# Performance work log

Hardware: AMD Instinct MI355X
Metric: run time of the kernel (lower is better)

The kernel has to match this reference:

```python
import jax, jax.numpy as jnp
import numpy as np

B, S, D, H = 4, 1024, 1024, 16
HS = D // H  # head_size = 64


def setup_inputs() -> dict:
    key = jax.random.key(0)
    ks = jax.random.split(key, 6)
    scale = 1.0 / np.sqrt(D)
    data = jax.random.normal(ks[0], (B, S, D), dtype=jnp.float32)
    # Per-head projection weights, stacked: [H, D, HS] (no bias, per nn.Linear(bias=False))
    Wq = jax.random.normal(ks[1], (H, D, HS), dtype=jnp.float32) * scale
    Wk = jax.random.normal(ks[2], (H, D, HS), dtype=jnp.float32) * scale
    Wv = jax.random.normal(ks[3], (H, D, HS), dtype=jnp.float32) * scale
    # Output projection: [H*HS, D] plus bias [D]
    Wo = jax.random.normal(ks[4], (H * HS, D), dtype=jnp.float32) * scale
    bo = jax.random.normal(ks[5], (D,), dtype=jnp.float32) * 0.01
    return {"data": data, "Wq": Wq, "Wk": Wk, "Wv": Wv, "Wo": Wo, "bo": bo}


def reference(data, Wq, Wk, Wv, Wo, bo):
    b, s, d = data.shape
    # Per-head Q/K/V projections (self-attention: encoder_data = data)
    q = jnp.einsum('bsd,hde->bhse', data, Wq)  # [B,H,S,HS]
    k = jnp.einsum('bsd,hde->bhse', data, Wk)
    v = jnp.einsum('bsd,hde->bhse', data, Wv)
    # NOTE: original scales by sqrt(embedding_dimension), not sqrt(head_size)
    scores = jnp.einsum('bhse,bhte->bhst', q, k) / jnp.sqrt(jnp.asarray(d, dtype=data.dtype))
    # causal mask (tril of block_size, sliced to [S, S])
    causal = jnp.tril(jnp.ones((s, s), dtype=bool))
    scores = jnp.where(causal, scores, -jnp.inf)
    attn = jax.nn.softmax(scores, axis=-1)  # dropout rate 0.0 -> identity
    out = jnp.einsum('bhst,bhte->bhse', attn, v)  # [B,H,S,HS]
    # concat heads along feature dim (head order matches ModuleList order)
    out = out.transpose(0, 2, 1, 3).reshape(b, s, -1)  # [B,S,H*HS]
    return out @ Wo + bo
```

## Files before the change

kernel.cpp:

```cpp
#include <hip/hip_runtime.h>
#include <hip/hip_bf16.h>
#include <stdint.h>

#define NEG_SENTINEL (-1e30f)

typedef short s16x8 __attribute__((ext_vector_type(8)));
typedef float f32x4 __attribute__((ext_vector_type(4)));
typedef float f32x16 __attribute__((ext_vector_type(16)));

__device__ __forceinline__ ushort f2bf(float f) {
  union { float f; uint32_t u; } v; v.f = f;
  uint32_t u = v.u;
  u += 0x7fffu + ((u >> 16) & 1u);
  return (ushort)(u >> 16);
}
__device__ __forceinline__ ushort f2bf_rn(float f) {
  union { float f; uint32_t u; } v; v.f = f;
  return (ushort)((v.u + 0x8000u) >> 16);
}

__device__ __forceinline__ uint32_t pk_bf16(float lo, float hi) {
  uint32_t r;
  asm("v_cvt_pk_bf16_f32 %0, %1, %2" : "=v"(r) : "v"(lo), "v"(hi));
  return r;
}

__device__ __forceinline__ void async_ld16(ushort* lds, const ushort* g) {
  __builtin_amdgcn_global_load_lds(
      (const __attribute__((address_space(1))) uint32_t*)g,
      (__attribute__((address_space(3))) uint32_t*)lds, 16, 0, 0);
}

__global__ __launch_bounds__(256) void convert_f32_bf16(
    const float* __restrict__ src, ushort* __restrict__ dst) {
  long i = ((long)blockIdx.x * 256 + threadIdx.x) * 8;
  float4 a = *(const float4*)(src + i);
  float4 b = *(const float4*)(src + i + 4);
  union { ushort u[8]; uint4 v; } o;
  o.u[0] = f2bf(a.x); o.u[1] = f2bf(a.y); o.u[2] = f2bf(a.z); o.u[3] = f2bf(a.w);
  o.u[4] = f2bf(b.x); o.u[5] = f2bf(b.y); o.u[6] = f2bf(b.z); o.u[7] = f2bf(b.w);
  *(uint4*)(dst + i) = o.v;
}

__global__ __launch_bounds__(256) void transpose_w3(
    const float* __restrict__ Wq, const float* __restrict__ Wk,
    const float* __restrict__ Wv, ushort* __restrict__ WTall) {
  const int z = blockIdx.z;
  const int matsel = z >> 4;
  const float* src = (matsel == 0 ? Wq : (matsel == 1 ? Wk : Wv)) +
                     (long)(z & 15) * 65536;
  ushort* dst = WTall + (long)z * 65536;
  const int it = blockIdx.y;
  __shared__ __align__(16) ushort tile[64 * 72];
  const int tid = threadIdx.x;
#pragma unroll
  for (int p = 0; p < 4; ++p) {
    int chunk = tid + p * 256;
    int r = chunk >> 4, c0 = (chunk & 15) * 4;
    float4 f = *(const float4*)(src + (long)(it * 64 + r) * 64 + c0);
    union { ushort u[4]; uint2 v; } o;
    o.u[0] = f2bf(f.x); o.u[1] = f2bf(f.y); o.u[2] = f2bf(f.z); o.u[3] = f2bf(f.w);
    *(uint2*)&tile[r * 72 + c0] = o.v;
  }
  __syncthreads();
#pragma unroll
  for (int p = 0; p < 2; ++p) {
    int chunk = tid + p * 256;
    int r = chunk >> 3, c0 = (chunk & 7) * 8;
    union { ushort u[8]; uint4 v; } tmp;
#pragma unroll
    for (int k2 = 0; k2 < 8; ++k2) tmp.u[k2] = tile[(c0 + k2) * 72 + r];
    *(uint4*)(dst + (long)r * 1024 + it * 64 + c0) = tmp.v;
  }
}

__global__ __launch_bounds__(256) void transpose_cvt(
    const float* __restrict__ src, ushort* __restrict__ dst) {
  const int jt = blockIdx.x;
  const int it = blockIdx.y;
  __shared__ __align__(16) ushort tile[64 * 72];
  const int tid = threadIdx.x;
#pragma unroll
  for (int p = 0; p < 4; ++p) {
    int chunk = tid + p * 256;
    int r = chunk >> 4, c0 = (chunk & 15) * 4;
    float4 f = *(const float4*)(src + (long)(it * 64 + r) * 1024 + jt * 64 + c0);
    union { ushort u[4]; uint2 v; } o;
    o.u[0] = f2bf(f.x); o.u[1] = f2bf(f.y); o.u[2] = f2bf(f.z); o.u[3] = f2bf(f.w);
    *(uint2*)&tile[r * 72 + c0] = o.v;
  }
  __syncthreads();
#pragma unroll
  for (int p = 0; p < 2; ++p) {
    int chunk = tid + p * 256;
    int r = chunk >> 3, c0 = (chunk & 7) * 8;
    union { ushort u[8]; uint4 v; } tmp;
#pragma unroll
    for (int k2 = 0; k2 < 8; ++k2) tmp.u[k2] = tile[(c0 + k2) * 72 + r];
    *(uint4*)(dst + (long)(jt * 64 + r) * 1024 + it * 64 + c0) = tmp.v;
  }
}

__device__ __forceinline__ void gemm_core_128x128(
    const ushort* __restrict__ A, const ushort* __restrict__ BT,
    ushort* As, ushort* Bs, f32x4 acc[4][4]) {
  const int tid = threadIdx.x;
  const int lane = tid & 63, w = tid >> 6, quad = lane >> 4, l15 = lane & 15;
  const int wm = w >> 1, wn = w & 1;
  for (int k0 = 0; k0 < 1024; k0 += 64) {
#pragma unroll
    for (int p = 0; p < 4; ++p) {
      int c = tid + p * 256;
      int r = c >> 3, c8 = (c & 7) * 8;
      async_ld16(As + c * 8, A + (long)r * 1024 + k0 + c8);
      async_ld16(Bs + c * 8, BT + (long)r * 1024 + k0 + c8);
    }
    __syncthreads();
#pragma unroll
    for (int kk = 0; kk < 64; kk += 32) {
      s16x8 af[4], bfr[4];
#pragma unroll
      for (int mi = 0; mi < 4; ++mi)
        af[mi] = *(const s16x8*)&As[(wm * 64 + mi * 16 + l15) * 64 + kk + quad * 8];
#pragma unroll
      for (int ni = 0; ni < 4; ++ni)
        bfr[ni] = *(const s16x8*)&Bs[(wn * 64 + ni * 16 + l15) * 64 + kk + quad * 8];
#pragma unroll
      for (int mi = 0; mi < 4; ++mi)
#pragma unroll
        for (int ni = 0; ni < 4; ++ni)
          acc[mi][ni] = __builtin_amdgcn_mfma_f32_16x16x32_bf16(
              af[mi], bfr[ni], acc[mi][ni], 0, 0, 0);
    }
    __syncthreads();
  }
}

#define BAR() do { asm volatile("" ::: "memory"); \
  __builtin_amdgcn_s_barrier(); \
  asm volatile("" ::: "memory"); } while (0)
#define LGKM0() do { asm volatile("s_waitcnt lgkmcnt(0)" ::: "memory"); \
  __builtin_amdgcn_sched_barrier(0); } while (0)
#define STAGE2(LDSB, G) do { \
  async_ld16((LDSB) + o0, (G) + so0); \
  async_ld16((LDSB) + o0 + 4096, (G) + so0 + 65536); } while (0)
#define LD_A(PA, MIB) do { \
  _Pragma("unroll") for (int dm = 0; dm < 4; ++dm) { \
    afr[dm][0] = *(const s16x8*)((PA) + ((MIB) + dm) * 1024); \
    afr[dm][1] = *(const s16x8*)((PA) + ((MIB) + dm) * 1024 + 512); } } while (0)
#define LD_B(PB, NIB) do { \
  _Pragma("unroll") for (int dn = 0; dn < 2; ++dn) { \
    bfr[(NIB) + dn][0] = *(const s16x8*)((PB) + ((NIB) + dn) * 1024); \
    bfr[(NIB) + dn][1] = *(const s16x8*)((PB) + ((NIB) + dn) * 1024 + 512); } } while (0)
#define MFMA_Q(MIB, NIB) do { \
  __builtin_amdgcn_s_setprio(1); \
  _Pragma("unroll") for (int kg = 0; kg < 2; ++kg) \
    _Pragma("unroll") for (int dm = 0; dm < 4; ++dm) \
      _Pragma("unroll") for (int dn = 0; dn < 2; ++dn) \
        acc[(MIB) + dm][(NIB) + dn] = __builtin_amdgcn_mfma_f32_16x16x32_bf16( \
            afr[dm][kg], bfr[(NIB) + dn][kg], acc[(MIB) + dm][(NIB) + dn], 0, 0, 0); \
  __builtin_amdgcn_s_setprio(0); } while (0)

__global__ __launch_bounds__(512, 2) void qkv_proj256(
    const ushort* __restrict__ dataB, const ushort* __restrict__ WTall,
    ushort* __restrict__ QKV) {
  __shared__ __align__(16) ushort smem[65536];
  const int tid = threadIdx.x;
  const int lane = tid & 63, w = tid >> 6, quad = lane >> 4, l15 = lane & 15;
  const int wm = w >> 2, wn = w & 3;
  const int m0 = blockIdx.x * 256;
  const int n0 = blockIdx.y * 256;

  const int o0 = tid * 8;
  const int st_ = o0 >> 9, u_ = o0 & 511;
  const int u0_ = u_ ^ (((u_ >> 8) & 1) << 4);
  const long so0 = (long)((st_ >> 1) * 16 + (u0_ >> 5)) * 1024 +
                   (st_ & 1) * 32 + (u0_ & 31);

  const ushort* Ab = dataB + (long)m0 * 1024;
  const ushort* Bb = WTall + (long)n0 * 1024;

  const int alane = (l15 * 32 + quad * 8) ^ (((l15 >> 3) & 1) << 4);
  const ushort* pA0 = smem + wm * 8192 + alane;
  const ushort* pB0 = smem + 16384 + (wn >> 1) * 8192 + (wn & 1) * 4096 + alane;
  const ushort* pA1 = pA0 + 32768;
  const ushort* pB1 = pB0 + 32768;

  f32x4 acc[8][4];
  const f32x4 z = {0.f, 0.f, 0.f, 0.f};
#pragma unroll
  for (int mi = 0; mi < 8; ++mi)
#pragma unroll
    for (int ni = 0; ni < 4; ++ni) acc[mi][ni] = z;

  s16x8 afr[4][2];
  s16x8 bfr[4][2];

  STAGE2(smem + 16384, Bb);
  STAGE2(smem + 16384 + 8192, Bb + 131072);
  STAGE2(smem, Ab);
  STAGE2(smem + 8192, Ab + 131072);
  STAGE2(smem + 32768 + 16384, Bb + 64);
  STAGE2(smem + 32768 + 16384 + 8192, Bb + 131072 + 64);
  asm volatile("s_waitcnt vmcnt(4)" ::: "memory");
  BAR();

#pragma unroll 1
  for (int it = 0; it < 8; ++it) {
    const int t0k = it * 128;
    const bool sN = (it < 7);
    LD_A(pA0, 0); LD_B(pB0, 0);
    STAGE2(smem + 32768, Ab + t0k + 64);
    asm volatile("s_waitcnt lgkmcnt(8)" ::: "memory");
    BAR(); LGKM0();
    MFMA_Q(0, 0);
    BAR();
    LD_B(pB0, 2);
    STAGE2(smem + 32768 + 8192, Ab + 131072 + t0k + 64);
    BAR(); LGKM0();
    MFMA_Q(0, 2);
    BAR();
    LD_A(pA0, 4);
    if (sN) STAGE2(smem + 16384, Bb + t0k + 128);
    BAR(); LGKM0();
    MFMA_Q(4, 0);
    BAR();
    if (sN) STAGE2(smem + 16384 + 8192, Bb + 131072 + t0k + 128);
    BAR(); LGKM0();
    MFMA_Q(4, 2);
    if (sN) { asm volatile("s_waitcnt vmcnt(4)" ::: "memory"); }
    else    { asm volatile("s_waitcnt vmcnt(0)" ::: "memory"); }
    BAR();
    LD_A(pA1, 0); LD_B(pB1, 0);
    if (sN) STAGE2(smem, Ab + t0k + 128);
    asm volatile("s_waitcnt lgkmcnt(8)" ::: "memory");
    BAR(); LGKM0();
    MFMA_Q(0, 0);
    BAR();
    LD_B(pB1, 2);
    if (sN) STAGE2(smem + 8192, Ab + 131072 + t0k + 128);
    BAR(); LGKM0();
    MFMA_Q(0, 2);
    BAR();
    LD_A(pA1, 4);
    if (sN) STAGE2(smem + 32768 + 16384, Bb + t0k + 192);
    BAR(); LGKM0();
    MFMA_Q(4, 0);
    BAR();
    if (sN) STAGE2(smem + 32768 + 16384 + 8192, Bb + 131072 + t0k + 192);
    BAR(); LGKM0();
    MFMA_Q(4, 2);
    if (sN) {
      asm volatile("s_waitcnt vmcnt(4)" ::: "memory");
      BAR();
    }
  }

  const int matsel = n0 >> 10;
  const int bI = m0 >> 10, s0 = m0 & 1023;
  const int nloc0 = (n0 & 1023) + wn * 64;
  if (matsel < 2) {
    const float sc = (matsel == 0) ? 0.04508422f : 1.0f;
    ushort* base = QKV + (long)matsel * 4194304 + (long)bI * 1048576;
#pragma unroll
    for (int mi = 0; mi < 8; ++mi) {
#pragma unroll
      for (int ni = 0; ni < 4; ++ni) {
        int n = nloc0 + ni * 16 + l15;
        int h = n >> 6, e = n & 63;
        int sb = s0 + wm * 128 + mi * 16 + quad * 4;
        ushort* p = base + (long)h * 65536 + (sb >> 5) * 2048 + (e >> 4) * 512 +
                    ((e >> 3) & 1) * 256 + (sb & 31) * 8 + (e & 7);
#pragma unroll
        for (int i = 0; i < 4; ++i)
          p[i * 8] = f2bf(acc[mi][ni][i] * sc);
      }
    }
  } else {
    ushort* base = QKV + 8388608 + (long)bI * 1048576;
#pragma unroll
    for (int mi = 0; mi < 8; ++mi) {
#pragma unroll
      for (int ni = 0; ni < 4; ++ni) {
        int n = nloc0 + ni * 16 + l15;
        int h = n >> 6, e = n & 63;
        int sb = s0 + wm * 128 + mi * 16 + quad * 4;
        union { ushort u[4]; uint2 v; } o;
#pragma unroll
        for (int i = 0; i < 4; ++i) o.u[i] = f2bf(acc[mi][ni][i]);
        *(uint2*)(base + (long)h * 65536 + (sb >> 5) * 2048 +
                  ((e >> 5) + 2 * ((sb >> 4) & 1)) * 512 +
                  ((e & 31) + 32 * ((sb >> 3) & 1)) * 8 + (sb & 7)) = o.v;
      }
    }
  }
}

__global__ __launch_bounds__(256) void out_proj(
    const ushort* __restrict__ Ocat, const ushort* __restrict__ WoT,
    const float* __restrict__ bo, float* __restrict__ out) {
  __shared__ __align__(16) ushort As[128 * 64];
  __shared__ __align__(16) ushort Bs[128 * 64];
  const int m0 = blockIdx.x * 128;
  const int n0 = blockIdx.y * 128;
  f32x4 acc[4][4];
  const f32x4 z = {0.f, 0.f, 0.f, 0.f};
#pragma unroll
  for (int mi = 0; mi < 4; ++mi)
#pragma unroll
    for (int ni = 0; ni < 4; ++ni) acc[mi][ni] = z;
  gemm_core_128x128(Ocat + (long)m0 * 1024, WoT + (long)n0 * 1024, As, Bs, acc);

  const int tid = threadIdx.x;
  const int lane = tid & 63, w = tid >> 6, quad = lane >> 4, l15 = lane & 15;
  const int wm = w >> 1, wn = w & 1;
#pragma unroll
  for (int mi = 0; mi < 4; ++mi) {
#pragma unroll
    for (int ni = 0; ni < 4; ++ni) {
#pragma unroll
      for (int i = 0; i < 4; ++i) {
        int m = m0 + wm * 64 + mi * 16 + quad * 4 + i;
        int n = n0 + wn * 64 + ni * 16 + l15;
        out[(long)m * 1024 + n] = acc[mi][ni][i] + bo[n];
      }
    }
  }
}

__global__ __launch_bounds__(256, 2) void attn_kernel(
    const ushort* __restrict__ QKV, ushort* __restrict__ Ocat) {
  const int x = blockIdx.x;
  const int tid = threadIdx.x;
  const int w = tid >> 6;
  const int lane = tid & 63, l31 = lane & 31, hi = lane >> 5;
  const int c = (x < 256) ? (31 - (x >> 4)) : ((x - 256) >> 4);
  const int bh = (x & 15) * 4 + w;
  const int b = bh >> 4, h = bh & 15;
  const int q0 = c * 32;

  const ushort* Qp = QKV + (long)bh * 65536;
  const ushort* Kp = QKV + 4194304 + (long)bh * 65536;
  const ushort* VTp = QKV + 8388608 + (long)bh * 65536;

  s16x8 qf[4];
#pragma unroll
  for (int es = 0; es < 4; ++es)
    qf[es] = *(const s16x8*)(Qp + c * 2048 + es * 512 + lane * 8);

  f32x16 oacc0, oacc1;
#pragma unroll
  for (int r = 0; r < 16; ++r) { oacc0[r] = 0.f; oacc1[r] = 0.f; }
  float l_part = 0.f;
  const int nsub = c + 1;

  s16x8 kc[4], vc[4], kn[4], vn[4];
#pragma unroll
  for (int es = 0; es < 4; ++es)
    kc[es] = *(const s16x8*)(Kp + es * 512 + lane * 8);
#pragma unroll
  for (int t = 0; t < 4; ++t)
    vc[t] = *(const s16x8*)(VTp + t * 512 + lane * 8);

  for (int s = 0;; ++s) {
    const bool last = (s + 1 >= nsub);
    if (!last) {
#pragma unroll
      for (int es = 0; es < 4; ++es)
        kn[es] = *(const s16x8*)(Kp + (s + 1) * 2048 + es * 512 + lane * 8);
#pragma unroll
      for (int t = 0; t < 4; ++t)
        vn[t] = *(const s16x8*)(VTp + (s + 1) * 2048 + t * 512 + lane * 8);
    }
    f32x16 sacc;
#pragma unroll
    for (int r = 0; r < 16; ++r) sacc[r] = 0.f;
#pragma unroll
    for (int es = 0; es < 4; ++es)
      sacc = __builtin_amdgcn_mfma_f32_32x32x16_bf16(kc[es], qf[es], sacc,
                                                     0, 0, 0);
    if (s == c) {
#pragma unroll
      for (int r = 0; r < 16; ++r) {
        int kvoff = (r & 3) + 8 * (r >> 2) + 4 * hi;
        if (kvoff > l31) sacc[r] = NEG_SENTINEL;
      }
    }
    float ex[16];
#pragma unroll
    for (int r = 0; r < 16; ++r) { ex[r] = exp2f(sacc[r]); l_part += ex[r]; }
    uint32_t xw[8], yw[8];
#pragma unroll
    for (int k = 0; k < 8; ++k) xw[k] = pk_bf16(ex[2 * k], ex[2 * k + 1]);
#pragma unroll
    for (int k = 0; k < 8; ++k)
      yw[k] = (uint32_t)__shfl_xor((int)xw[k], 32, 64);
#pragma unroll
    for (int win = 0; win < 2; ++win) {
      const int bs = 4 * win;
      union { uint32_t u[4]; s16x8 v; } pa;
      pa.u[0] = hi ? yw[bs + 2] : xw[bs + 0];
      pa.u[1] = hi ? yw[bs + 3] : xw[bs + 1];
      pa.u[2] = hi ? xw[bs + 2] : yw[bs + 0];
      pa.u[3] = hi ? xw[bs + 3] : yw[bs + 1];
      oacc0 = __builtin_amdgcn_mfma_f32_32x32x16_bf16(pa.v, vc[win * 2 + 0],
                                                      oacc0, 0, 0, 0);
      oacc1 = __builtin_amdgcn_mfma_f32_32x32x16_bf16(pa.v, vc[win * 2 + 1],
                                                      oacc1, 0, 0, 0);
    }
    if (last) break;
#pragma unroll
    for (int es = 0; es < 4; ++es) kc[es] = kn[es];
#pragma unroll
    for (int t = 0; t < 4; ++t) vc[t] = vn[t];
  }

  float l_tot = l_part + __shfl_xor(l_part, 32, 64);

  ushort* Ob = Ocat + ((long)(b * 1024 + q0) * 1024) + h * 64;
#pragma unroll
  for (int r = 0; r < 16; ++r) {
    int qloc = (r & 3) + 8 * (r >> 2) + 4 * hi;
    float lv = __shfl(l_tot, qloc, 64);
    float linv = __builtin_amdgcn_rcpf(lv > 1e-30f ? lv : 1.0f);
    Ob[(long)qloc * 1024 + l31] = f2bf_rn(oacc0[r] * linv);
    Ob[(long)qloc * 1024 + 32 + l31] = f2bf_rn(oacc1[r] * linv);
  }
}

extern "C" void kernel_launch(void* const* d_in, const int* in_sizes, int n_in,
                              void* d_out, int out_size, void* d_ws, size_t ws_size,
                              hipStream_t stream) {
  const float* data = (const float*)d_in[0];
  const float* Wq = (const float*)d_in[1];
  const float* Wk = (const float*)d_in[2];
  const float* Wv = (const float*)d_in[3];
  const float* Wo = (const float*)d_in[4];
  const float* bo = (const float*)d_in[5];
  float* out = (float*)d_out;

  ushort* ws = (ushort*)d_ws;
  ushort* QKV = ws;
  ushort* dataB = ws + 12582912;
  ushort* Ocat = ws + 16777216;
  ushort* WTall = ws + 20971520;
  ushort* WoT = ws + 20971520 + 3145728;

  dim3 blk(256);
  convert_f32_bf16<<<dim3(2048), blk, 0, stream>>>(data, dataB);
  transpose_w3<<<dim3(1, 16, 48), blk, 0, stream>>>(Wq, Wk, Wv, WTall);
  transpose_cvt<<<dim3(16, 16), blk, 0, stream>>>(Wo, WoT);
  qkv_proj256<<<dim3(16, 12), dim3(512), 0, stream>>>(dataB, WTall, QKV);
  attn_kernel<<<dim3(512), dim3(256), 0, stream>>>(QKV, Ocat);
  out_proj<<<dim3(32, 8), blk, 0, stream>>>(Ocat, WoT, bo, out);
}
```

Baseline: 175.2 us.

## Fuse prep kernels, double-buffer out_proj loads, pair causal chunks in attention blocks

Merges the three input conversion and transpose kernels into a single prep_all launch to cut launch overhead. Rewrites out_proj with double-buffered LDS so async loads of the next K-tile overlap the MFMAs on the current one, at the cost of twice the shared memory. Changes attention to 512-thread blocks where warps 0-3 take a long causal chunk and warps 4-7 the complementary short one, balancing work per block and halving the grid.

```diff
diff --git a/kernel.cpp b/kernel.cpp
--- a/kernel.cpp
+++ b/kernel.cpp
@@ -31,108 +31,79 @@
       (__attribute__((address_space(3))) uint32_t*)lds, 16, 0, 0);
 }
 
-__global__ __launch_bounds__(256) void convert_f32_bf16(
-    const float* __restrict__ src, ushort* __restrict__ dst) {
-  long i = ((long)blockIdx.x * 256 + threadIdx.x) * 8;
-  float4 a = *(const float4*)(src + i);
-  float4 b = *(const float4*)(src + i + 4);
-  union { ushort u[8]; uint4 v; } o;
-  o.u[0] = f2bf(a.x); o.u[1] = f2bf(a.y); o.u[2] = f2bf(a.z); o.u[3] = f2bf(a.w);
-  o.u[4] = f2bf(b.x); o.u[5] = f2bf(b.y); o.u[6] = f2bf(b.z); o.u[7] = f2bf(b.w);
-  *(uint4*)(dst + i) = o.v;
-}
-
-__global__ __launch_bounds__(256) void transpose_w3(
-    const float* __restrict__ Wq, const float* __restrict__ Wk,
-    const float* __restrict__ Wv, ushort* __restrict__ WTall) {
-  const int z = blockIdx.z;
-  const int matsel = z >> 4;
-  const float* src = (matsel == 0 ? Wq : (matsel == 1 ? Wk : Wv)) +
-                     (long)(z & 15) * 65536;
-  ushort* dst = WTall + (long)z * 65536;
-  const int it = blockIdx.y;
+__global__ __launch_bounds__(256) void prep_all(
+    const float* __restrict__ data, const float* __restrict__ Wq,
+    const float* __restrict__ Wk, const float* __restrict__ Wv,
+    const float* __restrict__ Wo, ushort* __restrict__ dataB,
+    ushort* __restrict__ WTall, ushort* __restrict__ WoT) {
+  const int g = blockIdx.x;
+  const int tid = threadIdx.x;
   __shared__ __align__(16) ushort tile[64 * 72];
-  const int tid = threadIdx.x;
-#pragma unroll
-  for (int p = 0; p < 4; ++p) {
-    int chunk = tid + p * 256;
-    int r = chunk >> 4, c0 = (chunk & 15) * 4;
-    float4 f = *(const float4*)(src + (long)(it * 64 + r) * 64 + c0);
-    union { ushort u[4]; uint2 v; } o;
-    o.u[0] = f2bf(f.x); o.u[1] = f2bf(f.y); o.u[2] = f2bf(f.z); o.u[3] = f2bf(f.w);
-    *(uint2*)&tile[r * 72 + c0] = o.v;
-  }
-  __syncthreads();
-#pragma unroll
-  for (int p = 0; p < 2; ++p) {
-    int chunk = tid + p * 256;
-    int r = chunk >> 3, c0 = (chunk & 7) * 8;
-    union { ushort u[8]; uint4 v; } tmp;
-#pragma unroll
-    for (int k2 = 0; k2 < 8; ++k2) tmp.u[k2] = tile[(c0 + k2) * 72 + r];
-    *(uint4*)(dst + (long)r * 1024 + it * 64 + c0) = tmp.v;
-  }
-}
-
-__global__ __launch_bounds__(256) void transpose_cvt(
-    const float* __restrict__ src, ushort* __restrict__ dst) {
-  const int jt = blockIdx.x;
-  const int it = blockIdx.y;
-  __shared__ __align__(16) ushort tile[64 * 72];
-  const int tid = threadIdx.x;
-#pragma unroll
-  for (int p = 0; p < 4; ++p) {
-    int chunk = tid + p * 256;
-    int r = chunk >> 4, c0 = (chunk & 15) * 4;
-    float4 f = *(const float4*)(src + (long)(it * 64 + r) * 1024 + jt * 64 + c0);
-    union { ushort u[4]; uint2 v; } o;
-    o.u[0] = f2bf(f.x); o.u[1] = f2bf(f.y); o.u[2] = f2bf(f.z); o.u[3] = f2bf(f.w);
-    *(uint2*)&tile[r * 72 + c0] = o.v;
-  }
-  __syncthreads();
-#pragma unroll
-  for (int p = 0; p < 2; ++p) {
-    int chunk = tid + p * 256;
-    int r = chunk >> 3, c0 = (chunk & 7) * 8;
-    union { ushort u[8]; uint4 v; } tmp;
-#pragma unroll
-    for (int k2 = 0; k2 < 8; ++k2) tmp.u[k2] = tile[(c0 + k2) * 72 + r];
-    *(uint4*)(dst + (long)(jt * 64 + r) * 1024 + it * 64 + c0) = tmp.v;
-  }
-}
-
-__device__ __forceinline__ void gemm_core_128x128(
-    const ushort* __restrict__ A, const ushort* __restrict__ BT,
-    ushort* As, ushort* Bs, f32x4 acc[4][4]) {
-  const int tid = threadIdx.x;
-  const int lane = tid & 63, w = tid >> 6, quad = lane >> 4, l15 = lane & 15;
-  const int wm = w >> 1, wn = w & 1;
-  for (int k0 = 0; k0 < 1024; k0 += 64) {
+
+  if (g < 2048) {
+    long i = ((long)g * 256 + tid) * 8;
+    float4 a = *(const float4*)(data + i);
+    float4 b = *(const float4*)(data + i + 4);
+    union { ushort u[8]; uint4 v; } o;
+    o.u[0] = f2bf(a.x); o.u[1] = f2bf(a.y); o.u[2] = f2bf(a.z); o.u[3] = f2bf(a.w);
+    o.u[4] = f2bf(b.x); o.u[5] = f2bf(b.y); o.u[6] = f2bf(b.z); o.u[7] = f2bf(b.w);
+    *(uint4*)(dataB + i) = o.v;
+    return;
+  }
+
+  if (g < 2816) {
+    const int u = g - 2048;
+    const int z = u >> 4, it = u & 15;
+    const int matsel = z >> 4;
+    const float* src = (matsel == 0 ? Wq : (matsel == 1 ? Wk : Wv)) +
+                       (long)(z & 15) * 65536;
+    ushort* dst = WTall + (long)z * 65536;
 #pragma unroll
     for (int p = 0; p < 4; ++p) {
-      int c = tid + p * 256;
-      int r = c >> 3, c8 = (c & 7) * 8;
-      async_ld16(As + c * 8, A + (long)r * 1024 + k0 + c8);
-      async_ld16(Bs + c * 8, BT + (long)r * 1024 + k0 + c8);
+      int chunk = tid + p * 256;
+      int r = chunk >> 4, c0 = (chunk & 15) * 4;
+      float4 f = *(const float4*)(src + (long)(it * 64 + r) * 64 + c0);
+      union { ushort u2[4]; uint2 v; } o;
+      o.u2[0] = f2bf(f.x); o.u2[1] = f2bf(f.y);
+      o.u2[2] = f2bf(f.z); o.u2[3] = f2bf(f.w);
+      *(uint2*)&tile[r * 72 + c0] = o.v;
     }
     __syncthreads();
 #pragma unroll
-    for (int kk = 0; kk < 64; kk += 32) {
-      s16x8 af[4], bfr[4];
-#pragma unroll
-      for (int mi = 0; mi < 4; ++mi)
-        af[mi] = *(const s16x8*)&As[(wm * 64 + mi * 16 + l15) * 64 + kk + quad * 8];
-#pragma unroll
-      for (int ni = 0; ni < 4; ++ni)
-        bfr[ni] = *(const s16x8*)&Bs[(wn * 64 + ni * 16 + l15) * 64 + kk + quad * 8];
-#pragma unroll
-      for (int mi = 0; mi < 4; ++mi)
-#pragma unroll
-        for (int ni = 0; ni < 4; ++ni)
-          acc[mi][ni] = __builtin_amdgcn_mfma_f32_16x16x32_bf16(
-              af[mi], bfr[ni], acc[mi][ni], 0, 0, 0);
+    for (int p = 0; p < 2; ++p) {
+      int chunk = tid + p * 256;
+      int r = chunk >> 3, c0 = (chunk & 7) * 8;
+      union { ushort u2[8]; uint4 v; } tmp;
+#pragma unroll
+      for (int k2 = 0; k2 < 8; ++k2) tmp.u2[k2] = tile[(c0 + k2) * 72 + r];
+      *(uint4*)(dst + (long)r * 1024 + it * 64 + c0) = tmp.v;
+    }
+    return;
+  }
+
+  {
+    const int u = g - 2816;
+    const int jt = u & 15, it = u >> 4;
+#pragma unroll
+    for (int p = 0; p < 4; ++p) {
+      int chunk = tid + p * 256;
+      int r = chunk >> 4, c0 = (chunk & 15) * 4;
+      float4 f = *(const float4*)(Wo + (long)(it * 64 + r) * 1024 + jt * 64 + c0);
+      union { ushort u2[4]; uint2 v; } o;
+      o.u2[0] = f2bf(f.x); o.u2[1] = f2bf(f.y);
+      o.u2[2] = f2bf(f.z); o.u2[3] = f2bf(f.w);
+      *(uint2*)&tile[r * 72 + c0] = o.v;
     }
     __syncthreads();
+#pragma unroll
+    for (int p = 0; p < 2; ++p) {
+      int chunk = tid + p * 256;
+      int r = chunk >> 3, c0 = (chunk & 7) * 8;
+      union { ushort u2[8]; uint4 v; } tmp;
+#pragma unroll
+      for (int k2 = 0; k2 < 8; ++k2) tmp.u2[k2] = tile[(c0 + k2) * 72 + r];
+      *(uint4*)(WoT + (long)(jt * 64 + r) * 1024 + it * 64 + c0) = tmp.v;
+    }
   }
 }
 
@@ -299,21 +270,65 @@
 __global__ __launch_bounds__(256) void out_proj(
     const ushort* __restrict__ Ocat, const ushort* __restrict__ WoT,
     const float* __restrict__ bo, float* __restrict__ out) {
-  __shared__ __align__(16) ushort As[128 * 64];
-  __shared__ __align__(16) ushort Bs[128 * 64];
+  __shared__ __align__(16) ushort As[2][128 * 64];
+  __shared__ __align__(16) ushort Bs[2][128 * 64];
   const int m0 = blockIdx.x * 128;
   const int n0 = blockIdx.y * 128;
-  f32x4 acc[4][4];
-  const f32x4 z = {0.f, 0.f, 0.f, 0.f};
-#pragma unroll
-  for (int mi = 0; mi < 4; ++mi)
-#pragma unroll
-    for (int ni = 0; ni < 4; ++ni) acc[mi][ni] = z;
-  gemm_core_128x128(Ocat + (long)m0 * 1024, WoT + (long)n0 * 1024, As, Bs, acc);
-
   const int tid = threadIdx.x;
   const int lane = tid & 63, w = tid >> 6, quad = lane >> 4, l15 = lane & 15;
   const int wm = w >> 1, wn = w & 1;
+  const ushort* A = Ocat + (long)m0 * 1024;
+  const ushort* BT = WoT + (long)n0 * 1024;
+
+  f32x4 acc[4][4];
+  const f32x4 z = {0.f, 0.f, 0.f, 0.f};
+#pragma unroll
+  for (int mi = 0; mi < 4; ++mi)
+#pragma unroll
+    for (int ni = 0; ni < 4; ++ni) acc[mi][ni] = z;
+
+  const int sc_ = tid;
+#pragma unroll
+  for (int p = 0; p < 4; ++p) {
+    int c = sc_ + p * 256;
+    int r = c >> 3, c8 = (c & 7) * 8;
+    async_ld16(&As[0][c * 8], A + (long)r * 1024 + c8);
+    async_ld16(&Bs[0][c * 8], BT + (long)r * 1024 + c8);
+  }
+  __syncthreads();
+
+#pragma unroll 1
+  for (int t = 0; t < 16; ++t) {
+    const int cur = t & 1;
+    if (t < 15) {
+      const int k0 = (t + 1) * 64;
+#pragma unroll
+      for (int p = 0; p < 4; ++p) {
+        int c = sc_ + p * 256;
+        int r = c >> 3, c8 = (c & 7) * 8;
+        async_ld16(&As[cur ^ 1][c * 8], A + (long)r * 1024 + k0 + c8);
+        async_ld16(&Bs[cur ^ 1][c * 8], BT + (long)r * 1024 + k0 + c8);
+      }
+    }
+#pragma unroll
+    for (int kk = 0; kk < 64; kk += 32) {
+      s16x8 af[4], bfr[4];
+#pragma unroll
+      for (int mi = 0; mi < 4; ++mi)
+        af[mi] = *(const s16x8*)&As[cur][(wm * 64 + mi * 16 + l15) * 64 + kk + quad * 8];
+#pragma unroll
+      for (int ni = 0; ni < 4; ++ni)
+        bfr[ni] = *(const s16x8*)&Bs[cur][(wn * 64 + ni * 16 + l15) * 64 + kk + quad * 8];
+#pragma unroll
+      for (int mi = 0; mi < 4; ++mi)
+#pragma unroll
+        for (int ni = 0; ni < 4; ++ni)
+          acc[mi][ni] = __builtin_amdgcn_mfma_f32_16x16x32_bf16(
+              af[mi], bfr[ni], acc[mi][ni], 0, 0, 0);
+    }
+    __syncthreads();
+  }
+
 #pragma unroll
   for (int mi = 0; mi < 4; ++mi) {
 #pragma unroll
@@ -328,14 +343,14 @@
   }
 }
 
-__global__ __launch_bounds__(256, 2) void attn_kernel(
+__global__ __launch_bounds__(512, 2) void attn_kernel(
     const ushort* __restrict__ QKV, ushort* __restrict__ Ocat) {
   const int x = blockIdx.x;
   const int tid = threadIdx.x;
   const int w = tid >> 6;
   const int lane = tid & 63, l31 = lane & 31, hi = lane >> 5;
-  const int c = (x < 256) ? (31 - (x >> 4)) : ((x - 256) >> 4);
-  const int bh = (x & 15) * 4 + w;
+  const int c = (w < 4) ? (31 - (x >> 4)) : (x >> 4);
+  const int bh = (x & 15) * 4 + (w & 3);
   const int b = bh >> 4, h = bh & 15;
   const int q0 = c * 32;
 
@@ -446,11 +461,9 @@
   ushort* WTall = ws + 20971520;
   ushort* WoT = ws + 20971520 + 3145728;
 
-  dim3 blk(256);
-  convert_f32_bf16<<<dim3(2048), blk, 0, stream>>>(data, dataB);
-  transpose_w3<<<dim3(1, 16, 48), blk, 0, stream>>>(Wq, Wk, Wv, WTall);
-  transpose_cvt<<<dim3(16, 16), blk, 0, stream>>>(Wo, WoT);
+  prep_all<<<dim3(3072), dim3(256), 0, stream>>>(data, Wq, Wk, Wv, Wo,
+                                                 dataB, WTall, WoT);
   qkv_proj256<<<dim3(16, 12), dim3(512), 0, stream>>>(dataB, WTall, QKV);
-  attn_kernel<<<dim3(512), dim3(256), 0, stream>>>(QKV, Ocat);
-  out_proj<<<dim3(32, 8), blk, 0, stream>>>(Ocat, WoT, bo, out);
-}
+  attn_kernel<<<dim3(256), dim3(512), 0, stream>>>(QKV, Ocat);
+  out_proj<<<dim3(32, 8), dim3(256), 0, stream>>>(Ocat, WoT, bo, out);
+}
```

Measured after the change: 174.6 us. About the same (-0.4%).
